# Kernel tuning notes

Hardware: AMD Instinct MI355X
Metric: run time of the kernel (lower is better)

## Reference

```python
import jax, jax.numpy as jnp
import numpy as np

N = 100000
E = 1600000
D = 128

def _degrees(idx, n):
    d = jax.ops.segment_sum(jnp.ones(idx.shape[0], jnp.float32), idx, num_segments=n)
    return jnp.clip(d, 1.0)

def _gconv(feat, src, dst, W, b, residual, act):
    n = feat.shape[0]
    norm_out = _degrees(src, n) ** -0.5            # [N] out-degree norm
    h = feat * norm_out[:, None]                   # scale src features
    msgs = h[src]                                  # gather [E, D]
    agg = jax.ops.segment_sum(msgs, dst, num_segments=n)  # scatter-sum [N, D]
    rst = agg @ W.T + b                            # dense linear
    norm_in = _degrees(dst, n) ** -0.5             # [N] in-degree norm
    rst = rst * norm_in[:, None]
    if residual:
        rst = rst + feat                           # identity residual (in==out)
    if act:
        rst = jax.nn.relu(rst)
    return rst

def setup_inputs() -> dict:
    key = jax.random.key(0)
    ks = jax.random.split(key, 10)
    feat = jax.random.normal(ks[0], (N, D), jnp.float32)
    src = jax.random.randint(ks[1], (E,), 0, N)
    dst = jax.random.randint(ks[2], (E,), 0, N)
    s = 1.0 / np.sqrt(D)
    W1 = jax.random.uniform(ks[3], (D, D), jnp.float32, -s, s)
    b1 = jax.random.uniform(ks[4], (D,), jnp.float32, -s, s)
    W2 = jax.random.uniform(ks[5], (D, D), jnp.float32, -s, s)
    b2 = jax.random.uniform(ks[6], (D,), jnp.float32, -s, s)
    W3 = jax.random.uniform(ks[7], (D, D), jnp.float32, -s, s)
    b3 = jax.random.uniform(ks[8], (D,), jnp.float32, -s, s)
    return {"feat": feat, "src": src, "dst": dst,
            "W1": W1, "b1": b1, "W2": W2, "b2": b2, "W3": W3, "b3": b3}

def reference(feat, src, dst, W1, b1, W2, b2, W3, b3):
    # 3-layer GCN, dropout=0, norm=None, encoding=False:
    # layers 0,1: residual + relu; layer 2: no residual, no activation
    h = _gconv(feat, src, dst, W1, b1, residual=True, act=True)
    h = _gconv(h, src, dst, W2, b2, residual=True, act=True)
    h = _gconv(h, src, dst, W3, b3, residual=False, act=False)
    return h
```

## Files before the change

kernel.cpp:

```cpp
#include <hip/hip_runtime.h>

#define NN 100000
#define EE 1600000
#define DD 128
#define NB 512
#define CAP 4608
#define CHUNK 8192

typedef __attribute__((ext_vector_type(8))) short short8v;
typedef __attribute__((ext_vector_type(4))) float f32x4;
typedef __attribute__((ext_vector_type(8))) unsigned short ushort8v;

static __device__ __forceinline__ unsigned short f2bf(float x) {
  unsigned u = __builtin_bit_cast(unsigned, x);
  return (unsigned short)((u + 0x7FFFu + ((u >> 16) & 1u)) >> 16);
}
static __device__ __forceinline__ float bf2f(unsigned short u) {
  return __builtin_bit_cast(float, (unsigned)u << 16);
}

__global__ __launch_bounds__(512) void initcur_k(int* __restrict__ cur_d,
                                                 int* __restrict__ cur_s) {
  int t = threadIdx.x;
  cur_d[t] = t * CAP;
  cur_s[t] = t * CAP;
}

__global__ __launch_bounds__(256) void split_k(const int* __restrict__ src,
                                               const int* __restrict__ dst,
                                               int* __restrict__ cur_d,
                                               int* __restrict__ cur_s,
                                               unsigned* __restrict__ tmp_d,
                                               unsigned char* __restrict__ tmp_s) {
  __shared__ int hd[NB], hs[NB], bd[NB], bs[NB];
  int t = threadIdx.x;
  int base = blockIdx.x * CHUNK;
  int end = base + CHUNK < EE ? base + CHUNK : EE;
  for (int b = t; b < NB; b += 256) { hd[b] = 0; hs[b] = 0; }
  __syncthreads();
  for (int i = base + t; i < end; i += 256) {
    atomicAdd(&hd[dst[i] >> 8], 1);
    atomicAdd(&hs[src[i] >> 8], 1);
  }
  __syncthreads();
  for (int b = t; b < NB; b += 256) {
    bd[b] = hd[b] ? atomicAdd(&cur_d[b], hd[b]) : 0;
    bs[b] = hs[b] ? atomicAdd(&cur_s[b], hs[b]) : 0;
    hd[b] = 0;
    hs[b] = 0;
  }
  __syncthreads();
  for (int i = base + t; i < end; i += 256) {
    int s = src[i];
    int d = dst[i];
    int bin = d >> 8;
    int r = atomicAdd(&hd[bin], 1);
    int pos = bd[bin] + r;
    if (pos < (bin + 1) * CAP) tmp_d[pos] = ((unsigned)(d & 255) << 17) | (unsigned)s;
    bin = s >> 8;
    r = atomicAdd(&hs[bin], 1);
    pos = bs[bin] + r;
    if (pos < (bin + 1) * CAP) tmp_s[pos] = (unsigned char)(s & 255);
  }
}

__global__ __launch_bounds__(512) void scan512_k(const int* __restrict__ cur_d,
                                                 int* __restrict__ dstart) {
  __shared__ int lds[512];
  int t = threadIdx.x;
  int v = cur_d[t] - t * CAP;
  v = v < CAP ? v : CAP;
  lds[t] = v;
  __syncthreads();
  int run = v;
  for (int off = 1; off < 512; off <<= 1) {
    int y = (t >= off) ? lds[t - off] : 0;
    __syncthreads();
    run += y;
    lds[t] = run;
    __syncthreads();
  }
  dstart[t] = run - v;
}

__global__ __launch_bounds__(256) void bucket_dst_k(const unsigned* __restrict__ tmp_d,
                                                    const int* __restrict__ cur_d,
                                                    const int* __restrict__ dstart,
                                                    int* __restrict__ csr,
                                                    int* __restrict__ row_s,
                                                    int* __restrict__ row_e,
                                                    float* __restrict__ norm_in) {
  __shared__ unsigned stage[CAP];
  __shared__ int h[256], sc[256], rk[256];
  int b = blockIdx.x;
  int t = threadIdx.x;
  int cnt = cur_d[b] - b * CAP;
  cnt = cnt < CAP ? cnt : CAP;
  int ds = dstart[b];
  for (int i = t; i < cnt; i += 256) stage[i] = tmp_d[b * CAP + i];
  h[t] = 0;
  __syncthreads();
  for (int i = t; i < cnt; i += 256) atomicAdd(&h[stage[i] >> 17], 1);
  __syncthreads();
  int v = h[t];
  sc[t] = v;
  __syncthreads();
  int run = v;
  for (int off = 1; off < 256; off <<= 1) {
    int y = (t >= off) ? sc[t - off] : 0;
    __syncthreads();
    run += y;
    sc[t] = run;
    __syncthreads();
  }
  int excl = run - v;
  int n = b * 256 + t;
  if (n < NN) {
    row_s[n] = ds + excl;
    row_e[n] = ds + excl + v;
    norm_in[n] = rsqrtf((float)(v > 1 ? v : 1));
  }
  rk[t] = excl;
  __syncthreads();
  for (int i = t; i < cnt; i += 256) {
    unsigned w = stage[i];
    int r = atomicAdd(&rk[w >> 17], 1);
    csr[ds + r] = (int)(w & 0x1FFFFu);
  }
}

__global__ __launch_bounds__(256) void bucket_src_k(const unsigned char* __restrict__ tmp_s,
                                                    const int* __restrict__ cur_s,
                                                    float* __restrict__ norm_out) {
  __shared__ int h[256];
  int b = blockIdx.x;
  int t = threadIdx.x;
  int cnt = cur_s[b] - b * CAP;
  cnt = cnt < CAP ? cnt : CAP;
  h[t] = 0;
  __syncthreads();
  const unsigned char* p = tmp_s + b * CAP;
  for (int i = t; i < cnt; i += 256) atomicAdd(&h[p[i]], 1);
  __syncthreads();
  int n = b * 256 + t;
  if (n < NN) norm_out[n] = rsqrtf((float)(h[t] > 1 ? h[t] : 1));
}

__global__ __launch_bounds__(256) void wconv_k(const float* __restrict__ w,
                                               unsigned short* __restrict__ o) {
  int i = blockIdx.x * 256 + threadIdx.x;
  float4 v = *reinterpret_cast<const float4*>(w + i * 4);
  ushort4 pk = make_ushort4(f2bf(v.x), f2bf(v.y), f2bf(v.z), f2bf(v.w));
  *reinterpret_cast<ushort4*>(o + i * 4) = pk;
}

__global__ __launch_bounds__(256) void hconv_k(const float* __restrict__ feat,
                                               const float* __restrict__ no,
                                               unsigned short* __restrict__ h) {
  int i = blockIdx.x * 256 + threadIdx.x;
  int node = i >> 4;
  int lane = i & 15;
  float n = no[node];
  const float* p = feat + node * DD + lane * 8;
  float4 a = *reinterpret_cast<const float4*>(p);
  float4 b = *reinterpret_cast<const float4*>(p + 4);
  ushort8v o;
  o[0] = f2bf(a.x * n); o[1] = f2bf(a.y * n); o[2] = f2bf(a.z * n); o[3] = f2bf(a.w * n);
  o[4] = f2bf(b.x * n); o[5] = f2bf(b.y * n); o[6] = f2bf(b.z * n); o[7] = f2bf(b.w * n);
  *reinterpret_cast<ushort8v*>(h + node * DD + lane * 8) = o;
}

__global__ __launch_bounds__(256) void layer_k(const unsigned short* __restrict__ h,
                                               const int* __restrict__ csr,
                                               const int* __restrict__ row_s,
                                               const int* __restrict__ row_e,
                                               const unsigned short* __restrict__ Wb,
                                               const float* __restrict__ bias,
                                               const float* __restrict__ nin,
                                               const float* __restrict__ nout,
                                               const float* __restrict__ resid,
                                               float* __restrict__ outp,
                                               unsigned short* __restrict__ hnext,
                                               int mode) {
  int wid = threadIdx.x >> 6;
  int lane = threadIdx.x & 63;
  int l15 = lane & 15;
  int kgrp = lane >> 4;
  int node = blockIdx.x * 64 + wid * 16 + l15;
  int nodec = node < NN ? node : NN - 1;

  int e0 = row_s[nodec];
  int e1 = row_e[nodec];
  float a0[8] = {0,0,0,0,0,0,0,0}, a1[8] = {0,0,0,0,0,0,0,0};
  float a2[8] = {0,0,0,0,0,0,0,0}, a3[8] = {0,0,0,0,0,0,0,0};
  const unsigned short* hb = h + kgrp * 8;
  int e = e0;
  for (; e + 2 <= e1; e += 2) {
    int s0 = csr[e];
    int s1 = csr[e + 1];
    const unsigned short* p0 = hb + (size_t)s0 * DD;
    const unsigned short* p1 = hb + (size_t)s1 * DD;
    ushort8v u0 = *reinterpret_cast<const ushort8v*>(p0);
    ushort8v u1 = *reinterpret_cast<const ushort8v*>(p0 + 32);
    ushort8v u2 = *reinterpret_cast<const ushort8v*>(p0 + 64);
    ushort8v u3 = *reinterpret_cast<const ushort8v*>(p0 + 96);
    ushort8v v0 = *reinterpret_cast<const ushort8v*>(p1);
    ushort8v v1 = *reinterpret_cast<const ushort8v*>(p1 + 32);
    ushort8v v2 = *reinterpret_cast<const ushort8v*>(p1 + 64);
    ushort8v v3 = *reinterpret_cast<const ushort8v*>(p1 + 96);
#pragma unroll
    for (int i = 0; i < 8; ++i) {
      a0[i] += bf2f(u0[i]) + bf2f(v0[i]);
      a1[i] += bf2f(u1[i]) + bf2f(v1[i]);
      a2[i] += bf2f(u2[i]) + bf2f(v2[i]);
      a3[i] += bf2f(u3[i]) + bf2f(v3[i]);
    }
  }
  if (e < e1) {
    int s0 = csr[e];
    const unsigned short* p0 = hb + (size_t)s0 * DD;
    ushort8v u0 = *reinterpret_cast<const ushort8v*>(p0);
    ushort8v u1 = *reinterpret_cast<const ushort8v*>(p0 + 32);
    ushort8v u2 = *reinterpret_cast<const ushort8v*>(p0 + 64);
    ushort8v u3 = *reinterpret_cast<const ushort8v*>(p0 + 96);
#pragma unroll
    for (int i = 0; i < 8; ++i) {
      a0[i] += bf2f(u0[i]);
      a1[i] += bf2f(u1[i]);
      a2[i] += bf2f(u2[i]);
      a3[i] += bf2f(u3[i]);
    }
  }
  short8v b0, b1, b2, b3;
#pragma unroll
  for (int i = 0; i < 8; ++i) {
    b0[i] = (short)f2bf(a0[i]);
    b1[i] = (short)f2bf(a1[i]);
    b2[i] = (short)f2bf(a2[i]);
    b3[i] = (short)f2bf(a3[i]);
  }

  float ninv = nin[nodec];
  float noutv = mode ? nout[nodec] : 0.f;

  for (int ct = 0; ct < 8; ++ct) {
    const unsigned short* wp = Wb + (size_t)(ct * 16 + l15) * DD + kgrp * 8;
    short8v w0 = *reinterpret_cast<const short8v*>(wp);
    short8v w1 = *reinterpret_cast<const short8v*>(wp + 32);
    short8v w2 = *reinterpret_cast<const short8v*>(wp + 64);
    short8v w3 = *reinterpret_cast<const short8v*>(wp + 96);
    f32x4 c = {0.f, 0.f, 0.f, 0.f};
    c = __builtin_amdgcn_mfma_f32_16x16x32_bf16(w0, b0, c, 0, 0, 0);
    c = __builtin_amdgcn_mfma_f32_16x16x32_bf16(w1, b1, c, 0, 0, 0);
    c = __builtin_amdgcn_mfma_f32_16x16x32_bf16(w2, b2, c, 0, 0, 0);
    c = __builtin_amdgcn_mfma_f32_16x16x32_bf16(w3, b3, c, 0, 0, 0);

    if (node < NN) {
      int j = ct * 16 + kgrp * 4;
      float4 bj = *reinterpret_cast<const float4*>(bias + j);
      size_t idx = (size_t)node * DD + j;
      float4 v;
      v.x = (c[0] + bj.x) * ninv;
      v.y = (c[1] + bj.y) * ninv;
      v.z = (c[2] + bj.z) * ninv;
      v.w = (c[3] + bj.w) * ninv;
      if (mode) {
        float4 rs = *reinterpret_cast<const float4*>(resid + idx);
        v.x = fmaxf(v.x + rs.x, 0.f);
        v.y = fmaxf(v.y + rs.y, 0.f);
        v.z = fmaxf(v.z + rs.z, 0.f);
        v.w = fmaxf(v.w + rs.w, 0.f);
        *reinterpret_cast<float4*>(outp + idx) = v;
        ushort4 hn = make_ushort4(f2bf(v.x * noutv), f2bf(v.y * noutv),
                                  f2bf(v.z * noutv), f2bf(v.w * noutv));
        *reinterpret_cast<ushort4*>(hnext + idx) = hn;
      } else {
        *reinterpret_cast<float4*>(outp + idx) = v;
      }
    }
  }
}

extern "C" void kernel_launch(void* const* d_in, const int* in_sizes, int n_in,
                              void* d_out, int out_size, void* d_ws, size_t ws_size,
                              hipStream_t stream) {
  const float* feat = (const float*)d_in[0];
  const int* src = (const int*)d_in[1];
  const int* dst = (const int*)d_in[2];
  const float* W1 = (const float*)d_in[3];
  const float* b1 = (const float*)d_in[4];
  const float* W2 = (const float*)d_in[5];
  const float* b2 = (const float*)d_in[6];
  const float* W3 = (const float*)d_in[7];
  const float* b3 = (const float*)d_in[8];
  float* out = (float*)d_out;

  int* row_s = (int*)d_ws;
  int* row_e = row_s + NN;
  float* norm_out = (float*)(row_e + NN);
  float* norm_in = norm_out + NN;
  int* cur_d = (int*)(norm_in + NN);
  int* cur_s = cur_d + NB;
  int* dstart = cur_s + NB;
  int* pad = dstart + NB;
  unsigned short* Wbf = (unsigned short*)pad;
  int* csr = (int*)(Wbf + 3 * 16384);
  unsigned short* hbuf = (unsigned short*)(csr + EE);
  unsigned short* hbuf2 = hbuf + (size_t)NN * DD;

  unsigned* tmp_d = (unsigned*)d_out;
  unsigned char* tmp_s = (unsigned char*)d_out + (size_t)NB * CAP * 4;

  initcur_k<<<1, 512, 0, stream>>>(cur_d, cur_s);
  split_k<<<(EE + CHUNK - 1) / CHUNK, 256, 0, stream>>>(src, dst, cur_d, cur_s, tmp_d, tmp_s);
  scan512_k<<<1, 512, 0, stream>>>(cur_d, dstart);
  bucket_dst_k<<<NB, 256, 0, stream>>>(tmp_d, cur_d, dstart, csr, row_s, row_e, norm_in);
  bucket_src_k<<<NB, 256, 0, stream>>>(tmp_s, cur_s, norm_out);

  wconv_k<<<16, 256, 0, stream>>>(W1, Wbf);
  wconv_k<<<16, 256, 0, stream>>>(W2, Wbf + 16384);
  wconv_k<<<16, 256, 0, stream>>>(W3, Wbf + 32768);
  hconv_k<<<6250, 256, 0, stream>>>(feat, norm_out, hbuf);

  const int GB = (NN + 63) / 64;
  layer_k<<<GB, 256, 0, stream>>>(hbuf, csr, row_s, row_e, Wbf, b1, norm_in,
                                  norm_out, feat, out, hbuf2, 1);
  layer_k<<<GB, 256, 0, stream>>>(hbuf2, csr, row_s, row_e, Wbf + 16384, b2, norm_in,
                                  norm_out, out, out, hbuf, 1);
  layer_k<<<GB, 256, 0, stream>>>(hbuf, csr, row_s, row_e, Wbf + 32768, b3, norm_in,
                                  norm_out, nullptr, out, nullptr, 0);
}
```

Measured before the change: 389.1 us.

## Sort nodes by in-degree and pair light/heavy groups per wavefront

Adds a counting sort of nodes by in-degree (histogram, scan, scatter into a permutation) so that each 16-node wave group holds nodes of similar degree, cutting divergence in the per-lane gather loop. Each wavefront then handles two groups taken from opposite ends of the sorted order to balance total work across waves. This costs three extra small kernels per call plus an indirection through perm. Output writes become scattered by node id instead of contiguous.

```diff
diff --git a/kernel.cpp b/kernel.cpp
--- a/kernel.cpp
+++ b/kernel.cpp
@@ -6,6 +6,8 @@
 #define NB 512
 #define CAP 4608
 #define CHUNK 8192
+#define NGRP 6250
+#define HALFG 3125
 
 typedef __attribute__((ext_vector_type(8))) short short8v;
 typedef __attribute__((ext_vector_type(4))) float f32x4;
@@ -20,10 +22,13 @@
 }
 
 __global__ __launch_bounds__(512) void initcur_k(int* __restrict__ cur_d,
-                                                 int* __restrict__ cur_s) {
+                                                 int* __restrict__ cur_s,
+                                                 int* __restrict__ ghist,
+                                                 int* __restrict__ bin_cur) {
   int t = threadIdx.x;
   cur_d[t] = t * CAP;
   cur_s[t] = t * CAP;
+  if (t < 64) { ghist[t] = 0; bin_cur[t] = 0; }
 }
 
 __global__ __launch_bounds__(256) void split_k(const int* __restrict__ src,
@@ -144,6 +149,62 @@
   __syncthreads();
   int n = b * 256 + t;
   if (n < NN) norm_out[n] = rsqrtf((float)(h[t] > 1 ? h[t] : 1));
+}
+
+__global__ __launch_bounds__(256) void deghist_k(const int* __restrict__ row_s,
+                                                 const int* __restrict__ row_e,
+                                                 int* __restrict__ ghist) {
+  __shared__ int lh[64];
+  int t = threadIdx.x;
+  int i = blockIdx.x * 256 + t;
+  if (t < 64) lh[t] = 0;
+  __syncthreads();
+  if (i < NN) {
+    int deg = row_e[i] - row_s[i];
+    atomicAdd(&lh[deg > 63 ? 63 : deg], 1);
+  }
+  __syncthreads();
+  if (t < 64 && lh[t]) atomicAdd(&ghist[t], lh[t]);
+}
+
+__global__ __launch_bounds__(64) void scan64_k(const int* __restrict__ ghist,
+                                               int* __restrict__ bin_start) {
+  int t = threadIdx.x;
+  int v = ghist[t];
+  int run = v;
+  for (int off = 1; off < 64; off <<= 1) {
+    int y = __shfl_up(run, off, 64);
+    if (t >= off) run += y;
+  }
+  bin_start[t] = run - v;
+}
+
+__global__ __launch_bounds__(256) void degsort_k(const int* __restrict__ row_s,
+                                                 const int* __restrict__ row_e,
+                                                 const int* __restrict__ bin_start,
+                                                 int* __restrict__ bin_cur,
+                                                 int* __restrict__ perm) {
+  __shared__ int lh[64], lbase[64], lrank[64];
+  int t = threadIdx.x;
+  int i = blockIdx.x * 256 + t;
+  if (t < 64) lh[t] = 0;
+  __syncthreads();
+  int bin = -1;
+  if (i < NN) {
+    int deg = row_e[i] - row_s[i];
+    bin = deg > 63 ? 63 : deg;
+    atomicAdd(&lh[bin], 1);
+  }
+  __syncthreads();
+  if (t < 64) {
+    lbase[t] = lh[t] ? atomicAdd(&bin_cur[t], lh[t]) : 0;
+    lrank[t] = 0;
+  }
+  __syncthreads();
+  if (i < NN) {
+    int r = atomicAdd(&lrank[bin], 1);
+    perm[bin_start[bin] + lbase[bin] + r] = i;
+  }
 }
 
 __global__ __launch_bounds__(256) void wconv_k(const float* __restrict__ w,
@@ -170,27 +231,23 @@
   *reinterpret_cast<ushort8v*>(h + node * DD + lane * 8) = o;
 }
 
-__global__ __launch_bounds__(256) void layer_k(const unsigned short* __restrict__ h,
-                                               const int* __restrict__ csr,
-                                               const int* __restrict__ row_s,
-                                               const int* __restrict__ row_e,
-                                               const unsigned short* __restrict__ Wb,
-                                               const float* __restrict__ bias,
-                                               const float* __restrict__ nin,
-                                               const float* __restrict__ nout,
-                                               const float* __restrict__ resid,
-                                               float* __restrict__ outp,
-                                               unsigned short* __restrict__ hnext,
-                                               int mode) {
-  int wid = threadIdx.x >> 6;
-  int lane = threadIdx.x & 63;
-  int l15 = lane & 15;
-  int kgrp = lane >> 4;
-  int node = blockIdx.x * 64 + wid * 16 + l15;
-  int nodec = node < NN ? node : NN - 1;
-
-  int e0 = row_s[nodec];
-  int e1 = row_e[nodec];
+__device__ __forceinline__ void do_group(int g, int l15, int kgrp,
+                                         const unsigned short* __restrict__ h,
+                                         const int* __restrict__ csr,
+                                         const int* __restrict__ row_s,
+                                         const int* __restrict__ row_e,
+                                         const int* __restrict__ perm,
+                                         const unsigned short* __restrict__ Wb,
+                                         const float* __restrict__ bias,
+                                         const float* __restrict__ nin,
+                                         const float* __restrict__ nout,
+                                         const float* __restrict__ resid,
+                                         float* __restrict__ outp,
+                                         unsigned short* __restrict__ hnext,
+                                         int mode) {
+  int node = perm[g * 16 + l15];
+  int e0 = row_s[node];
+  int e1 = row_e[node];
   float a0[8] = {0,0,0,0,0,0,0,0}, a1[8] = {0,0,0,0,0,0,0,0};
   float a2[8] = {0,0,0,0,0,0,0,0}, a3[8] = {0,0,0,0,0,0,0,0};
   const unsigned short* hb = h + kgrp * 8;
@@ -240,8 +297,8 @@
     b3[i] = (short)f2bf(a3[i]);
   }
 
-  float ninv = nin[nodec];
-  float noutv = mode ? nout[nodec] : 0.f;
+  float ninv = nin[node];
+  float noutv = mode ? nout[node] : 0.f;
 
   for (int ct = 0; ct < 8; ++ct) {
     const unsigned short* wp = Wb + (size_t)(ct * 16 + l15) * DD + kgrp * 8;
@@ -255,30 +312,53 @@
     c = __builtin_amdgcn_mfma_f32_16x16x32_bf16(w2, b2, c, 0, 0, 0);
     c = __builtin_amdgcn_mfma_f32_16x16x32_bf16(w3, b3, c, 0, 0, 0);
 
-    if (node < NN) {
-      int j = ct * 16 + kgrp * 4;
-      float4 bj = *reinterpret_cast<const float4*>(bias + j);
-      size_t idx = (size_t)node * DD + j;
-      float4 v;
-      v.x = (c[0] + bj.x) * ninv;
-      v.y = (c[1] + bj.y) * ninv;
-      v.z = (c[2] + bj.z) * ninv;
-      v.w = (c[3] + bj.w) * ninv;
-      if (mode) {
-        float4 rs = *reinterpret_cast<const float4*>(resid + idx);
-        v.x = fmaxf(v.x + rs.x, 0.f);
-        v.y = fmaxf(v.y + rs.y, 0.f);
-        v.z = fmaxf(v.z + rs.z, 0.f);
-        v.w = fmaxf(v.w + rs.w, 0.f);
-        *reinterpret_cast<float4*>(outp + idx) = v;
-        ushort4 hn = make_ushort4(f2bf(v.x * noutv), f2bf(v.y * noutv),
-                                  f2bf(v.z * noutv), f2bf(v.w * noutv));
-        *reinterpret_cast<ushort4*>(hnext + idx) = hn;
-      } else {
-        *reinterpret_cast<float4*>(outp + idx) = v;
-      }
+    int j = ct * 16 + kgrp * 4;
+    float4 bj = *reinterpret_cast<const float4*>(bias + j);
+    size_t idx = (size_t)node * DD + j;
+    float4 v;
+    v.x = (c[0] + bj.x) * ninv;
+    v.y = (c[1] + bj.y) * ninv;
+    v.z = (c[2] + bj.z) * ninv;
+    v.w = (c[3] + bj.w) * ninv;
+    if (mode) {
+      float4 rs = *reinterpret_cast<const float4*>(resid + idx);
+      v.x = fmaxf(v.x + rs.x, 0.f);
+      v.y = fmaxf(v.y + rs.y, 0.f);
+      v.z = fmaxf(v.z + rs.z, 0.f);
+      v.w = fmaxf(v.w + rs.w, 0.f);
+      *reinterpret_cast<float4*>(outp + idx) = v;
+      ushort4 hn = make_ushort4(f2bf(v.x * noutv), f2bf(v.y * noutv),
+                                f2bf(v.z * noutv), f2bf(v.w * noutv));
+      *reinterpret_cast<ushort4*>(hnext + idx) = hn;
+    } else {
+      *reinterpret_cast<float4*>(outp + idx) = v;
     }
   }
+}
+
+__global__ __launch_bounds__(256) void layer_k(const unsigned short* __restrict__ h,
+                                               const int* __restrict__ csr,
+                                               const int* __restrict__ row_s,
+                                               const int* __restrict__ row_e,
+                                               const int* __restrict__ perm,
+                                               const unsigned short* __restrict__ Wb,
+                                               const float* __restrict__ bias,
+                                               const float* __restrict__ nin,
+                                               const float* __restrict__ nout,
+                                               const float* __restrict__ resid,
+                                               float* __restrict__ outp,
+                                               unsigned short* __restrict__ hnext,
+                                               int mode) {
+  int wid = threadIdx.x >> 6;
+  int lane = threadIdx.x & 63;
+  int l15 = lane & 15;
+  int kgrp = lane >> 4;
+  int w = blockIdx.x * 4 + wid;
+  if (w >= HALFG) return;
+  do_group(w, l15, kgrp, h, csr, row_s, row_e, perm, Wb, bias, nin, nout,
+           resid, outp, hnext, mode);
+  do_group(NGRP - 1 - w, l15, kgrp, h, csr, row_s, row_e, perm, Wb, bias, nin,
+           nout, resid, outp, hnext, mode);
 }
 
 extern "C" void kernel_launch(void* const* d_in, const int* in_sizes, int n_in,
@@ -307,26 +387,34 @@
   int* csr = (int*)(Wbf + 3 * 16384);
   unsigned short* hbuf = (unsigned short*)(csr + EE);
   unsigned short* hbuf2 = hbuf + (size_t)NN * DD;
+  int* ghist = (int*)(hbuf2 + (size_t)NN * DD);
+  int* bin_cur = ghist + 64;
+  int* bin_start = bin_cur + 64;
+  int* perm = bin_start + 64;
 
   unsigned* tmp_d = (unsigned*)d_out;
   unsigned char* tmp_s = (unsigned char*)d_out + (size_t)NB * CAP * 4;
 
-  initcur_k<<<1, 512, 0, stream>>>(cur_d, cur_s);
+  initcur_k<<<1, 512, 0, stream>>>(cur_d, cur_s, ghist, bin_cur);
   split_k<<<(EE + CHUNK - 1) / CHUNK, 256, 0, stream>>>(src, dst, cur_d, cur_s, tmp_d, tmp_s);
   scan512_k<<<1, 512, 0, stream>>>(cur_d, dstart);
   bucket_dst_k<<<NB, 256, 0, stream>>>(tmp_d, cur_d, dstart, csr, row_s, row_e, norm_in);
   bucket_src_k<<<NB, 256, 0, stream>>>(tmp_s, cur_s, norm_out);
 
+  deghist_k<<<(NN + 255) / 256, 256, 0, stream>>>(row_s, row_e, ghist);
+  scan64_k<<<1, 64, 0, stream>>>(ghist, bin_start);
+  degsort_k<<<(NN + 255) / 256, 256, 0, stream>>>(row_s, row_e, bin_start, bin_cur, perm);
+
   wconv_k<<<16, 256, 0, stream>>>(W1, Wbf);
   wconv_k<<<16, 256, 0, stream>>>(W2, Wbf + 16384);
   wconv_k<<<16, 256, 0, stream>>>(W3, Wbf + 32768);
   hconv_k<<<6250, 256, 0, stream>>>(feat, norm_out, hbuf);
 
-  const int GB = (NN + 63) / 64;
-  layer_k<<<GB, 256, 0, stream>>>(hbuf, csr, row_s, row_e, Wbf, b1, norm_in,
+  const int GB = (HALFG + 3) / 4;
+  layer_k<<<GB, 256, 0, stream>>>(hbuf, csr, row_s, row_e, perm, Wbf, b1, norm_in,
                                   norm_out, feat, out, hbuf2, 1);
-  layer_k<<<GB, 256, 0, stream>>>(hbuf2, csr, row_s, row_e, Wbf + 16384, b2, norm_in,
+  layer_k<<<GB, 256, 0, stream>>>(hbuf2, csr, row_s, row_e, perm, Wbf + 16384, b2, norm_in,
                                   norm_out, out, out, hbuf, 1);
-  layer_k<<<GB, 256, 0, stream>>>(hbuf, csr, row_s, row_e, Wbf + 32768, b3, norm_in,
+  layer_k<<<GB, 256, 0, stream>>>(hbuf, csr, row_s, row_e, perm, Wbf + 32768, b3, norm_in,
                                   norm_out, nullptr, out, nullptr, 0);
 }
```

Measured after the change: 448.9 us. +15.4%, slower.

## Split fused gather-GEMM layer into separate aggregate and GEMM kernels

Applied to the files above, without the earlier changes.

Each layer's neighbor aggregation now runs in its own kernel, with 16 lanes per node reading contiguous 16-byte row slices, and writes a bf16 aggregate buffer. A separate GEMM kernel then loads that buffer for the MFMA transform and epilogue. The goal is better gather coalescing and occupancy than the register-heavy fused kernel, at the cost of an extra round trip through global memory for the intermediate buffer and additional launches.

```diff
diff --git a/kernel.cpp b/kernel.cpp
--- a/kernel.cpp
+++ b/kernel.cpp
@@ -170,10 +170,38 @@
   *reinterpret_cast<ushort8v*>(h + node * DD + lane * 8) = o;
 }
 
-__global__ __launch_bounds__(256) void layer_k(const unsigned short* __restrict__ h,
-                                               const int* __restrict__ csr,
-                                               const int* __restrict__ row_s,
-                                               const int* __restrict__ row_e,
+__global__ __launch_bounds__(256) void aggregate_k(const unsigned short* __restrict__ h,
+                                                   const int* __restrict__ csr,
+                                                   const int* __restrict__ row_s,
+                                                   const int* __restrict__ row_e,
+                                                   unsigned short* __restrict__ aggout) {
+  int node = (blockIdx.x * 256 + threadIdx.x) >> 4;
+  int lane = threadIdx.x & 15;
+  int e0 = row_s[node];
+  int e1 = row_e[node];
+  float acc[8] = {0.f, 0.f, 0.f, 0.f, 0.f, 0.f, 0.f, 0.f};
+  int e = e0;
+  for (; e + 2 <= e1; e += 2) {
+    int s0 = csr[e];
+    int s1 = csr[e + 1];
+    ushort8v u = *reinterpret_cast<const ushort8v*>(h + (size_t)s0 * DD + lane * 8);
+    ushort8v v = *reinterpret_cast<const ushort8v*>(h + (size_t)s1 * DD + lane * 8);
+#pragma unroll
+    for (int i = 0; i < 8; ++i) acc[i] += bf2f(u[i]) + bf2f(v[i]);
+  }
+  if (e < e1) {
+    int s0 = csr[e];
+    ushort8v u = *reinterpret_cast<const ushort8v*>(h + (size_t)s0 * DD + lane * 8);
+#pragma unroll
+    for (int i = 0; i < 8; ++i) acc[i] += bf2f(u[i]);
+  }
+  ushort8v o;
+#pragma unroll
+  for (int i = 0; i < 8; ++i) o[i] = f2bf(acc[i]);
+  *reinterpret_cast<ushort8v*>(aggout + (size_t)node * DD + lane * 8) = o;
+}
+
+__global__ __launch_bounds__(256) void gemm2_k(const unsigned short* __restrict__ A,
                                                const unsigned short* __restrict__ Wb,
                                                const float* __restrict__ bias,
                                                const float* __restrict__ nin,
@@ -189,56 +217,11 @@
   int node = blockIdx.x * 64 + wid * 16 + l15;
   int nodec = node < NN ? node : NN - 1;
 
-  int e0 = row_s[nodec];
-  int e1 = row_e[nodec];
-  float a0[8] = {0,0,0,0,0,0,0,0}, a1[8] = {0,0,0,0,0,0,0,0};
-  float a2[8] = {0,0,0,0,0,0,0,0}, a3[8] = {0,0,0,0,0,0,0,0};
-  const unsigned short* hb = h + kgrp * 8;
-  int e = e0;
-  for (; e + 2 <= e1; e += 2) {
-    int s0 = csr[e];
-    int s1 = csr[e + 1];
-    const unsigned short* p0 = hb + (size_t)s0 * DD;
-    const unsigned short* p1 = hb + (size_t)s1 * DD;
-    ushort8v u0 = *reinterpret_cast<const ushort8v*>(p0);
-    ushort8v u1 = *reinterpret_cast<const ushort8v*>(p0 + 32);
-    ushort8v u2 = *reinterpret_cast<const ushort8v*>(p0 + 64);
-    ushort8v u3 = *reinterpret_cast<const ushort8v*>(p0 + 96);
-    ushort8v v0 = *reinterpret_cast<const ushort8v*>(p1);
-    ushort8v v1 = *reinterpret_cast<const ushort8v*>(p1 + 32);
-    ushort8v v2 = *reinterpret_cast<const ushort8v*>(p1 + 64);
-    ushort8v v3 = *reinterpret_cast<const ushort8v*>(p1 + 96);
-#pragma unroll
-    for (int i = 0; i < 8; ++i) {
-      a0[i] += bf2f(u0[i]) + bf2f(v0[i]);
-      a1[i] += bf2f(u1[i]) + bf2f(v1[i]);
-      a2[i] += bf2f(u2[i]) + bf2f(v2[i]);
-      a3[i] += bf2f(u3[i]) + bf2f(v3[i]);
-    }
-  }
-  if (e < e1) {
-    int s0 = csr[e];
-    const unsigned short* p0 = hb + (size_t)s0 * DD;
-    ushort8v u0 = *reinterpret_cast<const ushort8v*>(p0);
-    ushort8v u1 = *reinterpret_cast<const ushort8v*>(p0 + 32);
-    ushort8v u2 = *reinterpret_cast<const ushort8v*>(p0 + 64);
-    ushort8v u3 = *reinterpret_cast<const ushort8v*>(p0 + 96);
-#pragma unroll
-    for (int i = 0; i < 8; ++i) {
-      a0[i] += bf2f(u0[i]);
-      a1[i] += bf2f(u1[i]);
-      a2[i] += bf2f(u2[i]);
-      a3[i] += bf2f(u3[i]);
-    }
-  }
-  short8v b0, b1, b2, b3;
-#pragma unroll
-  for (int i = 0; i < 8; ++i) {
-    b0[i] = (short)f2bf(a0[i]);
-    b1[i] = (short)f2bf(a1[i]);
-    b2[i] = (short)f2bf(a2[i]);
-    b3[i] = (short)f2bf(a3[i]);
-  }
+  const unsigned short* bp = A + (size_t)nodec * DD + kgrp * 8;
+  short8v b0 = *reinterpret_cast<const short8v*>(bp);
+  short8v b1 = *reinterpret_cast<const short8v*>(bp + 32);
+  short8v b2 = *reinterpret_cast<const short8v*>(bp + 64);
+  short8v b3 = *reinterpret_cast<const short8v*>(bp + 96);
 
   float ninv = nin[nodec];
   float noutv = mode ? nout[nodec] : 0.f;
@@ -306,7 +289,7 @@
   unsigned short* Wbf = (unsigned short*)pad;
   int* csr = (int*)(Wbf + 3 * 16384);
   unsigned short* hbuf = (unsigned short*)(csr + EE);
-  unsigned short* hbuf2 = hbuf + (size_t)NN * DD;
+  unsigned short* aggb = hbuf + (size_t)NN * DD;
 
   unsigned* tmp_d = (unsigned*)d_out;
   unsigned char* tmp_s = (unsigned char*)d_out + (size_t)NB * CAP * 4;
@@ -322,11 +305,11 @@
   wconv_k<<<16, 256, 0, stream>>>(W3, Wbf + 32768);
   hconv_k<<<6250, 256, 0, stream>>>(feat, norm_out, hbuf);
 
-  const int GB = (NN + 63) / 64;
-  layer_k<<<GB, 256, 0, stream>>>(hbuf, csr, row_s, row_e, Wbf, b1, norm_in,
-                                  norm_out, feat, out, hbuf2, 1);
-  layer_k<<<GB, 256, 0, stream>>>(hbuf2, csr, row_s, row_e, Wbf + 16384, b2, norm_in,
-                                  norm_out, out, out, hbuf, 1);
-  layer_k<<<GB, 256, 0, stream>>>(hbuf, csr, row_s, row_e, Wbf + 32768, b3, norm_in,
-                                  norm_out, nullptr, out, nullptr, 0);
-}
+  const int GG = (NN + 63) / 64;
+  aggregate_k<<<6250, 256, 0, stream>>>(hbuf, csr, row_s, row_e, aggb);
+  gemm2_k<<<GG, 256, 0, stream>>>(aggb, Wbf, b1, norm_in, norm_out, feat, out, hbuf, 1);
+  aggregate_k<<<6250, 256, 0, stream>>>(hbuf, csr, row_s, row_e, aggb);
+  gemm2_k<<<GG, 256, 0, stream>>>(aggb, Wbf + 16384, b2, norm_in, norm_out, out, out, hbuf, 1);
+  aggregate_k<<<6250, 256, 0, stream>>>(hbuf, csr, row_s, row_e, aggb);
+  gemm2_k<<<GG, 256, 0, stream>>>(aggb, Wbf + 32768, b3, norm_in, norm_out, nullptr, out, nullptr, 0);
+}
```

Result: no change. 390.4 us (+0.3%).
